# Optimization experiments

Hardware: AMD Instinct MI355X
Metric: run time of the kernel (lower is better)

## Reference

```python
import jax, jax.numpy as jnp
import numpy as np

EPS_DIST = 1e-3   # Memory.eps
EPS_COS = 1e-7    # PairwiseCosine eps
MOMENTUM = 0.999  # Memory.momentum (see NOTE below)


def _forward(points, descriptors, mem_points, mem_descriptors, usage):
    B = points.shape[0]
    # ---- point_address: cdist(p=2) + argmin over the 500k-slot bank ----
    # addressing is pure index selection (torch.no_grad); stop_gradient avoids
    # spurious NaN from sqrt(0) in vjp while matching the original semantics
    pd = jax.lax.stop_gradient(points)
    md = jax.lax.stop_gradient(mem_points)
    d2 = (jnp.sum(pd * pd, -1)[:, None] + jnp.sum(md * md, -1)[None, :]
          - 2.0 * pd @ md.T)                                  # [B, N]
    dist = jnp.sqrt(jnp.maximum(d2, 0.0))
    idx = jnp.argmin(dist, axis=-1)                            # [B]
    mind = jnp.min(dist, axis=-1)
    mask = mind > EPS_DIST                                     # "new" landmarks
    # torch: idx[mask] = usage.topk(k=mask.sum(), largest=False).indices
    # jit-safe: take B lowest-usage slots, assign them in order to masked rows
    _, low_usage_idx = jax.lax.top_k(-usage, B)
    rank = jnp.clip(jnp.cumsum(mask) - 1, 0)
    idx = jnp.where(mask, low_usage_idx[rank], idx)
    # NOTE: original builds momentum as zeros_like(idx) (int64) then assigns
    # 0.999 into it, which truncates to 0 -> EMA degenerates to full overwrite.
    # Replicated faithfully.
    mom = jnp.zeros((B, 1), descriptors.dtype)
    # ---- write: usage bump + EMA scatter (momentum==0 -> overwrite) ----
    usage_new = usage.at[idx].add(1)
    mem_points2 = mem_points.at[idx].set(mem_points[idx] * mom + (1.0 - mom) * points)
    mem_desc2 = mem_descriptors.at[idx].set(mem_descriptors[idx] * mom + (1.0 - mom) * descriptors)
    written = mem_desc2[idx]                                   # [B, F]
    # ---- read: masked pairwise-cosine retrieval (argmax over valid slots) ----
    valid = usage_new > 0                                      # [N]
    xn = jnp.linalg.norm(descriptors, axis=-1, keepdims=True)  # [B,1]
    yn = jnp.linalg.norm(mem_desc2, axis=-1)                   # [N]
    sim = (descriptors @ mem_desc2.T) / jnp.maximum(xn * yn[None, :], EPS_COS)
    sim = jnp.where(valid[None, :], sim, -jnp.inf)             # mask invalid slots
    cos = jnp.max(sim, axis=-1)                                # [B]
    idx2 = jnp.argmax(sim, axis=-1)
    read_desc = mem_desc2[idx2]                                # [B, F]
    # pack write-output, read descriptors, and cosine scores into one array
    return jnp.concatenate([written, read_desc, cos[:, None]], axis=-1)  # [B, 2F+1]


def setup_inputs() -> dict:
    key = jax.random.key(0)
    k0, k1, k2, k3, k4 = jax.random.split(key, 5)
    B, N, F = 256, 500000, 256
    return {
        "points": jax.random.normal(k0, (B, 3), jnp.float32) * 5.0,
        "descriptors": jax.random.normal(k1, (B, F), jnp.float32),
        "mem_points": jax.random.normal(k2, (N, 3), jnp.float32) * 5.0,
        "mem_descriptors": jax.random.normal(k3, (N, F), jnp.float32),
        "usage": jax.random.randint(k4, (N,), 0, 3, jnp.int32),
    }


def reference(points, descriptors, mem_points, mem_descriptors, usage):
    return _forward(points, descriptors, mem_points, mem_descriptors, usage)
```

## Files before the change

kernel.cpp:

```cpp
#include <hip/hip_runtime.h>
#include <stdint.h>


typedef __attribute__((ext_vector_type(4))) float  float4_t;
typedef _Float16 half8 __attribute__((ext_vector_type(8)));

#define WS_GMIN   0
#define WS_CTRL   2048
#define WS_HIST   4096
#define WS_CAND   (4096 + 262144)
#define WS_LOWU   (266240 + 8192)
#define WS_FIDX   (274432 + 1024)
#define WS_WSRC   (275456 + 1024)
#define WS_XN     (276480 + 1024)
#define WS_BMP    (277504 + 1024)
#define WS_PART   (278528 + 65536)

__global__ void k_init(uint32_t* __restrict__ hist, uint32_t* __restrict__ bmp,
                       unsigned long long* __restrict__ gmin, uint32_t* __restrict__ ctrl){
    int i = blockIdx.x * 256 + threadIdx.x;
    if (i < 65536) hist[i] = 0u;
    if (i < 16384) bmp[i] = 0u;
    if (i < 256)   gmin[i] = ~0ull;
    if (i < 8)     ctrl[i] = 0u;
}

__global__ void k_nearest(const float* __restrict__ pts, const float* __restrict__ mpts,
                          unsigned long long* __restrict__ gmin, int N){
    int t = threadIdx.x;
    float qx = pts[t*3+0], qy = pts[t*3+1], qz = pts[t*3+2];
    int chunk = (N + (int)gridDim.x - 1) / (int)gridDim.x;
    int lo = blockIdx.x * chunk;
    int hi = lo + chunk; if (hi > N) hi = N;
    unsigned long long best = ~0ull;
    #pragma unroll 4
    for (int n = lo; n < hi; ++n){
        float sx = mpts[3*n+0], sy = mpts[3*n+1], sz = mpts[3*n+2];
        float dx = qx - sx, dy = qy - sy, dz = qz - sz;
        float d2 = dx*dx + dy*dy + dz*dz;
        unsigned long long key = ((unsigned long long)__float_as_uint(d2) << 32) | (unsigned)n;
        best = key < best ? key : best;
    }
    if (lo < hi) atomicMin(&gmin[t], best);
}

__global__ void k_hist(const int* __restrict__ usage, uint32_t* __restrict__ hist,
                       int N, int sh){
    int stride = (int)gridDim.x * (int)blockDim.x;
    for (int i = blockIdx.x * blockDim.x + threadIdx.x; i < N; i += stride){
        int u = usage[i]; u = u < 0 ? 0 : (u > 63 ? 63 : u);
        atomicAdd(&hist[u*1024 + (i >> sh)], 1u);
    }
}

__global__ void k_select1(const uint32_t* __restrict__ hist, uint32_t* __restrict__ ctrl,
                          int sh, int Bq){
    __shared__ uint32_t ps[64*16];
    __shared__ uint32_t rsum[64];
    __shared__ uint32_t scan[1024];
    __shared__ uint32_t s_us, s_kp;
    int tid = threadIdx.x;
    int u = tid >> 4, m = tid & 15;
    uint32_t p = 0;
    for (int c = 0; c < 64; ++c) p += hist[u*1024 + m + (c << 4)];
    ps[u*16 + m] = p;
    __syncthreads();
    if (tid < 64){
        uint32_t s = 0;
        for (int j = 0; j < 16; ++j) s += ps[tid*16 + j];
        rsum[tid] = s;
    }
    __syncthreads();
    if (tid == 0){
        uint32_t cum = 0, c0 = 0; int us = 63;
        for (int v = 0; v < 64; ++v){
            if (cum + rsum[v] >= (uint32_t)Bq){ us = v; c0 = cum; break; }
            cum += rsum[v];
        }
        s_us = (uint32_t)us; s_kp = (uint32_t)Bq - c0;
        ctrl[0] = (uint32_t)us; ctrl[2] = s_kp; ctrl[3] = 0u;
    }
    __syncthreads();
    uint32_t ustar = s_us, kp = s_kp;
    uint32_t v = hist[ustar*1024 + tid];
    scan[tid] = v; __syncthreads();
    for (int off = 1; off < 1024; off <<= 1){
        uint32_t add = (tid >= off) ? scan[tid - off] : 0u;
        __syncthreads();
        scan[tid] += add;
        __syncthreads();
    }
    uint32_t inc = scan[tid], exc = inc - v;
    if (inc >= kp && exc < kp) ctrl[1] = (uint32_t)((tid + 1) << sh);
}

__global__ void k_collect(const int* __restrict__ usage, uint32_t* __restrict__ ctrl,
                          unsigned long long* __restrict__ cand, int N){
    int ustar = (int)ctrl[0]; uint32_t T = ctrl[1];
    int stride = (int)gridDim.x * (int)blockDim.x;
    for (int i = blockIdx.x * blockDim.x + threadIdx.x; i < N; i += stride){
        int u = usage[i]; int uc = u < 0 ? 0 : (u > 63 ? 63 : u);
        bool take = (uc < ustar) || (uc == ustar && (uint32_t)i < T);
        if (take){
            uint32_t pos = atomicAdd(&ctrl[3], 1u);
            if (pos < 1024u)
                cand[pos] = ((unsigned long long)(uint32_t)u << 32) | (uint32_t)i;
        }
    }
}

__global__ void k_sort(const uint32_t* __restrict__ ctrl,
                       unsigned long long* __restrict__ cand, int* __restrict__ lowu){
    __shared__ unsigned long long sk[1024];
    int tid = threadIdx.x;
    uint32_t cnt = ctrl[3]; if (cnt > 1024u) cnt = 1024u;
    sk[tid] = (tid < (int)cnt) ? cand[tid] : ~0ull;
    __syncthreads();
    for (int k = 2; k <= 1024; k <<= 1)
        for (int j = k >> 1; j > 0; j >>= 1){
            int ixj = tid ^ j;
            if (ixj > tid){
                unsigned long long a = sk[tid], b = sk[ixj];
                bool up = ((tid & k) == 0);
                bool sw = up ? (a > b) : (a < b);
                if (sw){ sk[tid] = b; sk[ixj] = a; }
            }
            __syncthreads();
        }
    if (tid < 256) lowu[tid] = (int)(uint32_t)sk[tid];
}

__global__ void k_assign(const float* __restrict__ desc,
                         const unsigned long long* __restrict__ gmin,
                         const int* __restrict__ lowu,
                         int* __restrict__ fidx, int* __restrict__ wsrc,
                         float* __restrict__ xn, uint32_t* __restrict__ bmp){
    __shared__ int sc[256];
    __shared__ int sidx[256];
    int b = threadIdx.x;
    unsigned long long key = gmin[b];
    float d2 = __uint_as_float((uint32_t)(key >> 32));
    int amin = (int)(uint32_t)key;
    int mask = (d2 > 1e-6f) ? 1 : 0;
    sc[b] = mask; __syncthreads();
    for (int off = 1; off < 256; off <<= 1){
        int add = (b >= off) ? sc[b - off] : 0;
        __syncthreads();
        sc[b] += add;
        __syncthreads();
    }
    int rank = sc[b] - 1; rank = rank < 0 ? 0 : (rank > 255 ? 255 : rank);
    int fi = mask ? lowu[rank] : amin;
    sidx[b] = fi; __syncthreads();
    int lw = b;
    for (int b2 = b + 1; b2 < 256; ++b2) if (sidx[b2] == fi) lw = b2;
    fidx[b] = fi; wsrc[b] = lw;
    atomicOr(&bmp[fi >> 5], 1u << (fi & 31));
    const float4_t* rp = (const float4_t*)(desc + b*256);
    float s = 0.f;
    #pragma unroll 8
    for (int i = 0; i < 64; ++i){
        float4_t v = rp[i];
        s += v[0]*v[0] + v[1]*v[1] + v[2]*v[2] + v[3]*v[3];
    }
    xn[b] = sqrtf(s);
}

__global__ __launch_bounds__(256, 2) void k_main(
        const float* __restrict__ desc, const float* __restrict__ mdesc,
        const int* __restrict__ usage, const uint32_t* __restrict__ bmp,
        float2* __restrict__ part, int N){
    constexpr int PITCH = 260;
    __shared__ float lds[16 * PITCH];
    __shared__ float s_sq[16 * 17];
    __shared__ float s_ryn[16];
    __shared__ float s_bias[16];
    int tid  = threadIdx.x;
    int wave = tid >> 6, lane = tid & 63;
    int l15  = lane & 15, q4 = lane >> 4;

    half8 afrag[4][8];
    #pragma unroll
    for (int mt = 0; mt < 4; ++mt){
        int q = 64*wave + 16*mt + l15;
        const float* rowp = desc + q*256 + q4*8;
        #pragma unroll
        for (int k0 = 0; k0 < 8; ++k0){
            float4_t f0 = *(const float4_t*)(rowp + 32*k0);
            float4_t f1 = *(const float4_t*)(rowp + 32*k0 + 4);
            half8 h;
            h[0]=(_Float16)f0[0]; h[1]=(_Float16)f0[1]; h[2]=(_Float16)f0[2]; h[3]=(_Float16)f0[3];
            h[4]=(_Float16)f1[0]; h[5]=(_Float16)f1[1]; h[6]=(_Float16)f1[2]; h[7]=(_Float16)f1[3];
            afrag[mt][k0] = h;
        }
    }
    float runv[4][4]; uint32_t runi[4][4];
    #pragma unroll
    for (int a = 0; a < 4; ++a)
        #pragma unroll
        for (int r = 0; r < 4; ++r){ runv[a][r] = -3e38f; runi[a][r] = 0u; }

    int r = tid & 15, m = tid >> 4;
    int tiles = (N + 15) >> 4;
    for (int t = blockIdx.x; t < tiles; t += (int)gridDim.x){
        int slot0 = t << 4;
        int s = slot0 + r;
        __syncthreads();
        float sq = 0.f;
        {
            const float* gp = mdesc + (size_t)s * 256 + m*16;
            float* lp = lds + r*PITCH + m*16;
            if (s < N){
                #pragma unroll
                for (int c = 0; c < 4; ++c){
                    float4_t v = *(const float4_t*)(gp + 4*c);
                    sq += v[0]*v[0] + v[1]*v[1] + v[2]*v[2] + v[3]*v[3];
                    *(float4_t*)(lp + 4*c) = v;
                }
            } else {
                #pragma unroll
                for (int c = 0; c < 4; ++c) *(float4_t*)(lp + 4*c) = (float4_t){0.f,0.f,0.f,0.f};
            }
        }
        s_sq[r*17 + m] = sq;
        __syncthreads();
        if (tid < 16){
            float tot = 0.f;
            #pragma unroll
            for (int j = 0; j < 16; ++j) tot += s_sq[tid*17 + j];
            int ss = slot0 + tid;
            bool valid = (ss < N) && (usage[ss] > 0) && !((bmp[ss >> 5] >> (ss & 31)) & 1u);
            s_ryn[tid]  = (ss < N) ? rsqrtf(fmaxf(tot, 1e-30f)) : 0.f;
            s_bias[tid] = valid ? 0.f : -1e30f;
        }
        __syncthreads();

        float4_t acc[4];
        #pragma unroll
        for (int a = 0; a < 4; ++a) acc[a] = (float4_t){0.f,0.f,0.f,0.f};
        const float* bp = lds + l15*PITCH + q4*8;
        #pragma unroll
        for (int k0 = 0; k0 < 8; ++k0){
            float4_t b0 = *(const float4_t*)(bp + 32*k0);
            float4_t b1 = *(const float4_t*)(bp + 32*k0 + 4);
            half8 hb;
            hb[0]=(_Float16)b0[0]; hb[1]=(_Float16)b0[1]; hb[2]=(_Float16)b0[2]; hb[3]=(_Float16)b0[3];
            hb[4]=(_Float16)b1[0]; hb[5]=(_Float16)b1[1]; hb[6]=(_Float16)b1[2]; hb[7]=(_Float16)b1[3];
            #pragma unroll
            for (int mt = 0; mt < 4; ++mt)
                acc[mt] = __builtin_amdgcn_mfma_f32_16x16x32_f16(afrag[mt][k0], hb, acc[mt], 0, 0, 0);
        }
        float ryn  = s_ryn[l15];
        float bias = s_bias[l15];
        uint32_t sidx = (uint32_t)(slot0 + l15);
        #pragma unroll
        for (int mt = 0; mt < 4; ++mt)
            #pragma unroll
            for (int rr = 0; rr < 4; ++rr){
                float val = acc[mt][rr] * ryn + bias;
                if (val > runv[mt][rr]){ runv[mt][rr] = val; runi[mt][rr] = sidx; }
            }
    }
    #pragma unroll
    for (int mt = 0; mt < 4; ++mt)
        #pragma unroll
        for (int rr = 0; rr < 4; ++rr){
            float v = runv[mt][rr]; uint32_t ix = runi[mt][rr];
            for (int off = 1; off < 16; off <<= 1){
                float vo   = __shfl_xor(v, off, 64);
                uint32_t io = (uint32_t)__shfl_xor((int)ix, off, 64);
                if (vo > v || (vo == v && io < ix)){ v = vo; ix = io; }
            }
            if (l15 == 0){
                int q = 64*wave + 16*mt + q4*4 + rr;
                part[(size_t)blockIdx.x * 256 + q] = make_float2(v, __uint_as_float(ix));
            }
        }
}

__global__ void k_fin(const float* __restrict__ desc, const float* __restrict__ mdesc,
                      const float2* __restrict__ part, const int* __restrict__ fidx,
                      const int* __restrict__ wsrc, const float* __restrict__ xn,
                      float* __restrict__ out, int N, int NB){
    __shared__ float rv[256]; __shared__ int ri[256]; __shared__ int rs[256];
    int q = blockIdx.x, tid = threadIdx.x;
    int s_j = fidx[tid], r_j = wsrc[tid];
    const float4_t* qa = (const float4_t*)(desc + q*256);
    const float4_t* ra = (const float4_t*)(desc + r_j*256);
    float dot = 0.f;
    #pragma unroll 8
    for (int i = 0; i < 64; ++i){
        float4_t a = qa[i], b = ra[i];
        dot += a[0]*b[0] + a[1]*b[1] + a[2]*b[2] + a[3]*b[3];
    }
    float xq = xn[q];
    float bv = dot / fmaxf(xq * xn[r_j], 1e-7f);
    int bi = s_j, bs = r_j;
    float rxn = 1.f / xq;
    for (int p = tid; p < NB; p += 256){
        float2 e = part[(size_t)p * 256 + q];
        float val = e.x * rxn;
        int idx = (int)__float_as_uint(e.y);
        if (val > bv || (val == bv && idx < bi)){ bv = val; bi = idx; bs = -1; }
    }
    rv[tid] = bv; ri[tid] = bi; rs[tid] = bs;
    __syncthreads();
    for (int s = 128; s > 0; s >>= 1){
        if (tid < s){
            float v2 = rv[tid + s]; int i2 = ri[tid + s];
            if (v2 > rv[tid] || (v2 == rv[tid] && i2 < ri[tid])){
                rv[tid] = v2; ri[tid] = i2; rs[tid] = rs[tid + s];
            }
        }
        __syncthreads();
    }
    float win_v = rv[0]; int win_i = ri[0]; int win_s = rs[0];
    const float* wrow = desc + wsrc[q]*256;
    const float* rrow = (win_s >= 0) ? (desc + win_s*256) : (mdesc + (size_t)win_i * 256);
    size_t ob = (size_t)q * 513;
    out[ob + tid]       = wrow[tid];
    out[ob + 256 + tid] = rrow[tid];
    if (tid == 0) out[ob + 512] = win_v;
}

extern "C" void kernel_launch(void* const* d_in, const int* in_sizes, int n_in,
                              void* d_out, int out_size, void* d_ws, size_t ws_size,
                              hipStream_t stream){
    const float* pts   = (const float*)d_in[0];
    const float* desc  = (const float*)d_in[1];
    const float* mpts  = (const float*)d_in[2];
    const float* mdesc = (const float*)d_in[3];
    const int*   usage = (const int*)d_in[4];
    int N = in_sizes[4];

    char* ws = (char*)d_ws;
    unsigned long long* gmin = (unsigned long long*)(ws + WS_GMIN);
    uint32_t* ctrl = (uint32_t*)(ws + WS_CTRL);
    uint32_t* hist = (uint32_t*)(ws + WS_HIST);
    unsigned long long* cand = (unsigned long long*)(ws + WS_CAND);
    int*   lowu = (int*)(ws + WS_LOWU);
    int*   fidx = (int*)(ws + WS_FIDX);
    int*   wsrc = (int*)(ws + WS_WSRC);
    float* xn   = (float*)(ws + WS_XN);
    uint32_t* bmp = (uint32_t*)(ws + WS_BMP);
    float2* part  = (float2*)(ws + WS_PART);

    int sh = 9; while (((N - 1) >> sh) >= 1024) ++sh;
    int tiles = (N + 15) >> 4;
    int NB = 512;
    if (ws_size > (size_t)WS_PART){
        size_t avail = (ws_size - (size_t)WS_PART) / (256 * sizeof(float2));
        if ((size_t)NB > avail) NB = (int)avail;
    }
    if (NB > tiles) NB = tiles;
    if (NB < 1) NB = 1;

    k_init   <<<256, 256, 0, stream>>>(hist, bmp, gmin, ctrl);
    k_nearest<<<512, 256, 0, stream>>>(pts, mpts, gmin, N);
    k_hist   <<<1024, 256, 0, stream>>>(usage, hist, N, sh);
    k_select1<<<1, 1024, 0, stream>>>(hist, ctrl, sh, 256);
    k_collect<<<1024, 256, 0, stream>>>(usage, ctrl, cand, N);
    k_sort   <<<1, 1024, 0, stream>>>(ctrl, cand, lowu);
    k_assign <<<1, 256, 0, stream>>>(desc, gmin, lowu, fidx, wsrc, xn, bmp);
    k_main   <<<NB, 256, 0, stream>>>(desc, mdesc, usage, bmp, part, N);
    k_fin    <<<256, 256, 0, stream>>>(desc, mdesc, part, fidx, wsrc, xn,
                                       (float*)d_out, N, NB);
}
```

Measured before the change: 1.002 ms.

## Load memory tiles per wave directly from global, aggregate histogram atomics

The main cosine kernel drops the shared-memory staging and the three block barriers per tile. Each wave now loads its own 16-slot tile straight from global memory into MFMA operands, computes row norms with cross-lane shuffles, and writes partials in a q-major layout for the final reduction. The histogram kernel merges atomics for equal bins within a wave using ballot, and the nearest-point kernel gets more blocks. The direct global loads are strided per lane, which may coalesce worse than the old staged copy, and the number of partials grows to 2048 per query.

Measured after the change: 808.1 us. 19.4% less time.

```diff
diff --git a/kernel.cpp b/kernel.cpp
--- a/kernel.cpp
+++ b/kernel.cpp
@@ -47,9 +47,25 @@
 __global__ void k_hist(const int* __restrict__ usage, uint32_t* __restrict__ hist,
                        int N, int sh){
     int stride = (int)gridDim.x * (int)blockDim.x;
-    for (int i = blockIdx.x * blockDim.x + threadIdx.x; i < N; i += stride){
-        int u = usage[i]; u = u < 0 ? 0 : (u > 63 ? 63 : u);
-        atomicAdd(&hist[u*1024 + (i >> sh)], 1u);
+    int lane = threadIdx.x & 63;
+    for (int base = blockIdx.x * blockDim.x; base < N; base += stride){
+        int i = base + (int)threadIdx.x;
+        bool ok = i < N;
+        int u = 0, bin = 0;
+        if (ok){
+            u = usage[i]; u = u < 0 ? 0 : (u > 63 ? 63 : u);
+            bin = i >> sh;
+        }
+        unsigned long long rem = __ballot(ok);
+        while (rem){
+            int leader = __ffsll(rem) - 1;
+            int lu = __shfl(u,   leader, 64);
+            int lb = __shfl(bin, leader, 64);
+            unsigned long long match = __ballot(ok && u == lu && bin == lb) & rem;
+            if (lane == leader)
+                atomicAdd(&hist[lu*1024 + lb], (uint32_t)__popcll(match));
+            rem &= ~match;
+        }
     }
 }
 
@@ -169,15 +185,11 @@
 __global__ __launch_bounds__(256, 2) void k_main(
         const float* __restrict__ desc, const float* __restrict__ mdesc,
         const int* __restrict__ usage, const uint32_t* __restrict__ bmp,
-        float2* __restrict__ part, int N){
-    constexpr int PITCH = 260;
-    __shared__ float lds[16 * PITCH];
-    __shared__ float s_sq[16 * 17];
-    __shared__ float s_ryn[16];
-    __shared__ float s_bias[16];
+        float2* __restrict__ part, int N, int NW){
     int tid  = threadIdx.x;
     int wave = tid >> 6, lane = tid & 63;
     int l15  = lane & 15, q4 = lane >> 4;
+    int W = blockIdx.x * 4 + wave;
 
     half8 afrag[4][8];
     #pragma unroll
@@ -200,49 +212,32 @@
         #pragma unroll
         for (int r = 0; r < 4; ++r){ runv[a][r] = -3e38f; runi[a][r] = 0u; }
 
-    int r = tid & 15, m = tid >> 4;
     int tiles = (N + 15) >> 4;
-    for (int t = blockIdx.x; t < tiles; t += (int)gridDim.x){
-        int slot0 = t << 4;
-        int s = slot0 + r;
-        __syncthreads();
+    const float* pb = mdesc + (size_t)l15 * 256 + q4 * 8 + (size_t)W * (16 * 256);
+    size_t tstep = (size_t)NW * (16 * 256);
+
+    for (int t = W; t < tiles; t += NW){
+        int s = (t << 4) + l15;
+        bool sok = s < N;
+        int uval = sok ? usage[s] : 0;
+        uint32_t bw = sok ? bmp[s >> 5] : 0u;
+        const float* pc = pb; pb += tstep;
         float sq = 0.f;
-        {
-            const float* gp = mdesc + (size_t)s * 256 + m*16;
-            float* lp = lds + r*PITCH + m*16;
-            if (s < N){
-                #pragma unroll
-                for (int c = 0; c < 4; ++c){
-                    float4_t v = *(const float4_t*)(gp + 4*c);
-                    sq += v[0]*v[0] + v[1]*v[1] + v[2]*v[2] + v[3]*v[3];
-                    *(float4_t*)(lp + 4*c) = v;
-                }
+        float4_t acc[4];
+        #pragma unroll
+        for (int a = 0; a < 4; ++a) acc[a] = (float4_t){0.f,0.f,0.f,0.f};
+        #pragma unroll
+        for (int k0 = 0; k0 < 8; ++k0){
+            float4_t b0, b1;
+            if (sok){
+                b0 = *(const float4_t*)(pc + 32*k0);
+                b1 = *(const float4_t*)(pc + 32*k0 + 4);
             } else {
-                #pragma unroll
-                for (int c = 0; c < 4; ++c) *(float4_t*)(lp + 4*c) = (float4_t){0.f,0.f,0.f,0.f};
-            }
-        }
-        s_sq[r*17 + m] = sq;
-        __syncthreads();
-        if (tid < 16){
-            float tot = 0.f;
-            #pragma unroll
-            for (int j = 0; j < 16; ++j) tot += s_sq[tid*17 + j];
-            int ss = slot0 + tid;
-            bool valid = (ss < N) && (usage[ss] > 0) && !((bmp[ss >> 5] >> (ss & 31)) & 1u);
-            s_ryn[tid]  = (ss < N) ? rsqrtf(fmaxf(tot, 1e-30f)) : 0.f;
-            s_bias[tid] = valid ? 0.f : -1e30f;
-        }
-        __syncthreads();
-
-        float4_t acc[4];
-        #pragma unroll
-        for (int a = 0; a < 4; ++a) acc[a] = (float4_t){0.f,0.f,0.f,0.f};
-        const float* bp = lds + l15*PITCH + q4*8;
-        #pragma unroll
-        for (int k0 = 0; k0 < 8; ++k0){
-            float4_t b0 = *(const float4_t*)(bp + 32*k0);
-            float4_t b1 = *(const float4_t*)(bp + 32*k0 + 4);
+                b0 = (float4_t){0.f,0.f,0.f,0.f};
+                b1 = (float4_t){0.f,0.f,0.f,0.f};
+            }
+            sq += b0[0]*b0[0] + b0[1]*b0[1] + b0[2]*b0[2] + b0[3]*b0[3]
+                + b1[0]*b1[0] + b1[1]*b1[1] + b1[2]*b1[2] + b1[3]*b1[3];
             half8 hb;
             hb[0]=(_Float16)b0[0]; hb[1]=(_Float16)b0[1]; hb[2]=(_Float16)b0[2]; hb[3]=(_Float16)b0[3];
             hb[4]=(_Float16)b1[0]; hb[5]=(_Float16)b1[1]; hb[6]=(_Float16)b1[2]; hb[7]=(_Float16)b1[3];
@@ -250,9 +245,12 @@
             for (int mt = 0; mt < 4; ++mt)
                 acc[mt] = __builtin_amdgcn_mfma_f32_16x16x32_f16(afrag[mt][k0], hb, acc[mt], 0, 0, 0);
         }
-        float ryn  = s_ryn[l15];
-        float bias = s_bias[l15];
-        uint32_t sidx = (uint32_t)(slot0 + l15);
+        sq += __shfl_xor(sq, 16, 64);
+        sq += __shfl_xor(sq, 32, 64);
+        float ryn = rsqrtf(fmaxf(sq, 1e-30f));
+        bool valid = sok && (uval > 0) && !((bw >> (s & 31)) & 1u);
+        float bias = valid ? 0.f : -1e30f;
+        uint32_t sidx = (uint32_t)s;
         #pragma unroll
         for (int mt = 0; mt < 4; ++mt)
             #pragma unroll
@@ -273,7 +271,7 @@
             }
             if (l15 == 0){
                 int q = 64*wave + 16*mt + q4*4 + rr;
-                part[(size_t)blockIdx.x * 256 + q] = make_float2(v, __uint_as_float(ix));
+                part[(size_t)q * NW + W] = make_float2(v, __uint_as_float(ix));
             }
         }
 }
@@ -281,7 +279,7 @@
 __global__ void k_fin(const float* __restrict__ desc, const float* __restrict__ mdesc,
                       const float2* __restrict__ part, const int* __restrict__ fidx,
                       const int* __restrict__ wsrc, const float* __restrict__ xn,
-                      float* __restrict__ out, int N, int NB){
+                      float* __restrict__ out, int N, int NW){
     __shared__ float rv[256]; __shared__ int ri[256]; __shared__ int rs[256];
     int q = blockIdx.x, tid = threadIdx.x;
     int s_j = fidx[tid], r_j = wsrc[tid];
@@ -297,8 +295,8 @@
     float bv = dot / fmaxf(xq * xn[r_j], 1e-7f);
     int bi = s_j, bs = r_j;
     float rxn = 1.f / xq;
-    for (int p = tid; p < NB; p += 256){
-        float2 e = part[(size_t)p * 256 + q];
+    for (int p = tid; p < NW; p += 256){
+        float2 e = part[(size_t)q * NW + p];
         float val = e.x * rxn;
         int idx = (int)__float_as_uint(e.y);
         if (val > bv || (val == bv && idx < bi)){ bv = val; bi = idx; bs = -1; }
@@ -346,23 +344,20 @@
     float2* part  = (float2*)(ws + WS_PART);
 
     int sh = 9; while (((N - 1) >> sh) >= 1024) ++sh;
-    int tiles = (N + 15) >> 4;
-    int NB = 512;
-    if (ws_size > (size_t)WS_PART){
-        size_t avail = (ws_size - (size_t)WS_PART) / (256 * sizeof(float2));
-        if ((size_t)NB > avail) NB = (int)avail;
-    }
-    if (NB > tiles) NB = tiles;
-    if (NB < 1) NB = 1;
+
+    int NW = 2048;
+    while (NW > 8 && (size_t)WS_PART + (size_t)NW * 256 * sizeof(float2) > ws_size)
+        NW >>= 1;
+    int nb_main = NW / 4;
 
     k_init   <<<256, 256, 0, stream>>>(hist, bmp, gmin, ctrl);
-    k_nearest<<<512, 256, 0, stream>>>(pts, mpts, gmin, N);
+    k_nearest<<<1024, 256, 0, stream>>>(pts, mpts, gmin, N);
     k_hist   <<<1024, 256, 0, stream>>>(usage, hist, N, sh);
     k_select1<<<1, 1024, 0, stream>>>(hist, ctrl, sh, 256);
     k_collect<<<1024, 256, 0, stream>>>(usage, ctrl, cand, N);
     k_sort   <<<1, 1024, 0, stream>>>(ctrl, cand, lowu);
     k_assign <<<1, 256, 0, stream>>>(desc, gmin, lowu, fidx, wsrc, xn, bmp);
-    k_main   <<<NB, 256, 0, stream>>>(desc, mdesc, usage, bmp, part, N);
+    k_main   <<<nb_main, 256, 0, stream>>>(desc, mdesc, usage, bmp, part, N, NW);
     k_fin    <<<256, 256, 0, stream>>>(desc, mdesc, part, fidx, wsrc, xn,
-                                       (float*)d_out, N, NB);
-}
+                                       (float*)d_out, N, NW);
+}
```
